# Kernel tuning notes

Measured on AMD Instinct MI355X. Metric: run time of the kernel, lower is better.

The kernel has to match this reference:

```python
import jax, jax.numpy as jnp
import numpy as np

B, T_ENC, T_OUT = 64, 1024, 1000
N_MELS, ENC_D, DEC_H, ATTN_D = 80, 256, 256, 256


def setup_inputs() -> dict:
    key = jax.random.key(0)
    ks = jax.random.split(key, 24)

    def p(k, shape, scale=0.05):
        return jax.random.normal(k, shape, dtype=jnp.float32) * scale

    lengths = jax.random.randint(ks[0], (B,), T_ENC // 2, T_ENC + 1)
    enc_mask = (jnp.arange(T_ENC)[None, :] < lengths[:, None]).astype(jnp.float32)
    return {
        "enc_outputs": jax.random.normal(ks[1], (B, T_ENC, ENC_D), dtype=jnp.float32),
        "target_mel": jax.random.normal(ks[2], (B, T_OUT, N_MELS), dtype=jnp.float32),
        # attention params
        "W_enc": p(ks[3], (ATTN_D, ENC_D)), "b_enc": jnp.zeros((ATTN_D,), jnp.float32),
        "W_dec": p(ks[4], (ATTN_D, DEC_H)), "b_dec": jnp.zeros((ATTN_D,), jnp.float32),
        "v_w": p(ks[5], (1, ATTN_D)), "v_b": jnp.zeros((1,), jnp.float32),
        # prenet
        "pre_W1": p(ks[6], (DEC_H, N_MELS)), "pre_b1": jnp.zeros((DEC_H,), jnp.float32),
        "pre_W2": p(ks[7], (DEC_H, DEC_H)), "pre_b2": jnp.zeros((DEC_H,), jnp.float32),
        # LSTMCell (PyTorch gate order i, f, g, o)
        "W_ih": p(ks[8], (4 * DEC_H, DEC_H + ENC_D)), "W_hh": p(ks[9], (4 * DEC_H, DEC_H)),
        "b_ih": jnp.zeros((4 * DEC_H,), jnp.float32), "b_hh": jnp.zeros((4 * DEC_H,), jnp.float32),
        # output heads
        "mel_W": p(ks[10], (N_MELS, DEC_H + ENC_D)), "mel_b": jnp.zeros((N_MELS,), jnp.float32),
        "stop_W": p(ks[11], (1, DEC_H + ENC_D)), "stop_b": jnp.zeros((1,), jnp.float32),
        "enc_mask": enc_mask,
    }


def reference(enc_outputs, target_mel, W_enc, b_enc, W_dec, b_dec, v_w, v_b,
              pre_W1, pre_b1, pre_W2, pre_b2, W_ih, W_hh, b_ih, b_hh,
              mel_W, mel_b, stop_W, stop_b, enc_mask):
    Bsz = enc_outputs.shape[0]
    H = W_hh.shape[1]
    NEG = jnp.float32(-1e9)
    # precompute encoder projection once, as the original does
    attn_enc = jnp.einsum('bte,ae->bta', enc_outputs, W_enc) + b_enc  # (B, T_enc, A)
    # teacher forcing: input at step t is target_mel[t-1], zeros at t=0
    prev_inputs = jnp.concatenate(
        [jnp.zeros_like(target_mel[:, :1]), target_mel[:, :-1]], axis=1)
    xs = jnp.swapaxes(prev_inputs, 0, 1)  # (T_out, B, n_mels)

    def step(carry, prev):
        h, c = carry
        attn_dec = h @ W_dec.T + b_dec                                  # (B, A)
        energy = jnp.tanh(attn_enc + attn_dec[:, None, :]) @ v_w[0] + v_b[0]  # (B, T_enc)
        energy = jnp.where(enc_mask == 0, NEG, energy)
        attn = jax.nn.softmax(energy, axis=-1)
        context = jnp.einsum('bt,btd->bd', attn, enc_outputs)           # (B, enc_d)
        pre = jax.nn.relu(prev @ pre_W1.T + pre_b1)                     # dropout = identity (eval)
        pre = jax.nn.relu(pre @ pre_W2.T + pre_b2)
        x = jnp.concatenate([pre, context], axis=1)
        gates = x @ W_ih.T + b_ih + h @ W_hh.T + b_hh                   # (B, 4H)
        i, f, g, o = jnp.split(gates, 4, axis=1)
        c_new = jax.nn.sigmoid(f) * c + jax.nn.sigmoid(i) * jnp.tanh(g)
        h_new = jax.nn.sigmoid(o) * jnp.tanh(c_new)
        comb = jnp.concatenate([h_new, context], axis=1)
        mel = comb @ mel_W.T + mel_b
        stop = (comb @ stop_W.T + stop_b)[:, 0]
        return (h_new, c_new), (mel, stop)

    h0 = jnp.zeros((Bsz, H), dtype=enc_outputs.dtype)
    _, (mels, stops) = jax.lax.scan(step, (h0, h0), xs)
    return jnp.swapaxes(mels, 0, 1), jnp.swapaxes(stops, 0, 1)
```

## Files before the change

kernel.cpp:

```cpp
#include <hip/hip_runtime.h>
#include <hip/hip_bf16.h>

#define NMEL 80

typedef unsigned u32x4 __attribute__((ext_vector_type(4)));

__device__ __forceinline__ float bf2f(unsigned short u) {
  unsigned v = ((unsigned)u) << 16; float f; __builtin_memcpy(&f, &v, 4); return f;
}
__device__ __forceinline__ unsigned short f2bf_u(float f) {
  __hip_bfloat16 h = __float2bfloat16(f); unsigned short u; __builtin_memcpy(&u, &h, 2); return u;
}
__device__ __forceinline__ void unpk(unsigned u, float& lo, float& hi) {
  unsigned l = u << 16, h = u & 0xffff0000u;
  __builtin_memcpy(&lo, &l, 4); __builtin_memcpy(&hi, &h, 4);
}

constexpr size_t OFF_ATTNR = 0;
constexpr size_t SZ_ATTNR = (size_t)64 * 1024 * 256 * 2;
constexpr size_t OFF_ENCP = OFF_ATTNR + SZ_ATTNR;
constexpr size_t SZ_ENCP = (size_t)64 * 1024 * 256 * 2;
constexpr size_t OFF_PRE2 = OFF_ENCP + SZ_ENCP;
constexpr size_t SZ_PRE2 = (size_t)64000 * 256 * 2;
constexpr size_t OFF_WDT = OFF_PRE2 + SZ_PRE2;
constexpr size_t SZ_WDT = (size_t)65536 * 4;
constexpr size_t OFF_WHT = OFF_WDT + SZ_WDT;
constexpr size_t SZ_W1M = (size_t)262144 * 4;
constexpr size_t OFF_WCT = OFF_WHT + SZ_W1M;
constexpr size_t OFF_WPT = OFF_WCT + SZ_W1M;
constexpr size_t OFF_BIASG = OFF_WPT + SZ_W1M;
constexpr size_t SZ_BIASG = 1024 * 4;
constexpr size_t WS_NEED = OFF_BIASG + SZ_BIASG;

__global__ __launch_bounds__(256) void conv_encP(const float* __restrict__ enc,
                                                 u32x4* __restrict__ encP) {
  int idx = blockIdx.x * 256 + threadIdx.x;
  int b = idx >> 15, r = idx & 32767;
  int d8 = r >> 10, te = r & 1023;
  const float4* src = (const float4*)(enc + ((size_t)(b * 1024 + te)) * 256 + d8 * 8);
  float4 x0 = src[0], x1 = src[1];
  u32x4 o;
  o.x = (unsigned)f2bf_u(x0.x) | ((unsigned)f2bf_u(x0.y) << 16);
  o.y = (unsigned)f2bf_u(x0.z) | ((unsigned)f2bf_u(x0.w) << 16);
  o.z = (unsigned)f2bf_u(x1.x) | ((unsigned)f2bf_u(x1.y) << 16);
  o.w = (unsigned)f2bf_u(x1.z) | ((unsigned)f2bf_u(x1.w) << 16);
  encP[((size_t)(b * 32 + d8)) * 1024 + te] = o;
}

__global__ __launch_bounds__(256) void prep_w2(
    const float* __restrict__ W_dec, const float* __restrict__ W_hh,
    const float* __restrict__ W_ih, const float* __restrict__ b_ih,
    const float* __restrict__ b_hh,
    float* __restrict__ WdT, float* __restrict__ WhT,
    float* __restrict__ WcT, float* __restrict__ WpT, float* __restrict__ biasG) {
  int idx = blockIdx.x * 256 + threadIdx.x;
  if (idx < 65536) {
    int q = idx & 3, a = (idx >> 2) & 255, kq = idx >> 10;
    WdT[idx] = W_dec[(size_t)a * 256 + kq * 4 + q];
  } else if (idx < 327680) {
    int i = idx - 65536;
    int q = i & 3, g = (i >> 2) & 1023, kq = i >> 12;
    WhT[i] = W_hh[(size_t)g * 256 + kq * 4 + q];
  } else if (idx < 589824) {
    int i = idx - 327680;
    int q = i & 3, g = (i >> 2) & 1023, kq = i >> 12;
    WcT[i] = W_ih[(size_t)g * 512 + 256 + kq * 4 + q];
  } else if (idx < 851968) {
    int i = idx - 589824;
    int q = i & 3, g = (i >> 2) & 1023, kq = i >> 12;
    WpT[i] = W_ih[(size_t)g * 512 + kq * 4 + q];
  } else if (idx < 852992) {
    int g = idx - 851968;
    biasG[g] = b_ih[g] + b_hh[g];
  }
}

__global__ __launch_bounds__(256) void attn_gemm(const float* __restrict__ enc,
                                                 const float* __restrict__ W_enc,
                                                 const float* __restrict__ b_enc,
                                                 unsigned* __restrict__ attnR) {
  __shared__ unsigned short Alds[64 * 260];
  const int tid = threadIdx.x;
  const int row0 = blockIdx.x * 64;
  const int wv = tid >> 6, lane = tid & 63, nb = wv * 64;
  for (int idx = tid; idx < 64 * 256; idx += 256) {
    int r = idx >> 8, k = idx & 255;
    Alds[r * 260 + k] = f2bf_u(enc[(size_t)(row0 + r) * 256 + k]);
  }
  __syncthreads();
  float acc[64];
#pragma unroll
  for (int n = 0; n < 64; ++n) acc[n] = b_enc[nb + n];
  for (int k8 = 0; k8 < 256; k8 += 8) {
    ushort4 ua = *(const ushort4*)&Alds[lane * 260 + k8];
    ushort4 ub = *(const ushort4*)&Alds[lane * 260 + k8 + 4];
    float a0 = bf2f(ua.x), a1 = bf2f(ua.y), a2 = bf2f(ua.z), a3 = bf2f(ua.w);
    float a4 = bf2f(ub.x), a5 = bf2f(ub.y), a6 = bf2f(ub.z), a7 = bf2f(ub.w);
#pragma unroll
    for (int n = 0; n < 64; ++n) {
      const float4* wp = (const float4*)(W_enc + (size_t)(nb + n) * 256 + k8);
      float4 w0 = wp[0], w1 = wp[1];
      acc[n] = fmaf(a0, w0.x, acc[n]); acc[n] = fmaf(a1, w0.y, acc[n]);
      acc[n] = fmaf(a2, w0.z, acc[n]); acc[n] = fmaf(a3, w0.w, acc[n]);
      acc[n] = fmaf(a4, w1.x, acc[n]); acc[n] = fmaf(a5, w1.y, acc[n]);
      acc[n] = fmaf(a6, w1.z, acc[n]); acc[n] = fmaf(a7, w1.w, acc[n]);
    }
  }
  const float CE = 2.8853900817779268f;
  const int b = row0 >> 10;
  const int te_g = (row0 & 1023) + lane;
  const int sl = te_g >> 8, te_loc = te_g & 255;
#pragma unroll
  for (int n = 0; n < 64; n += 2) {
    int a = nb + n;
    unsigned pair = (unsigned)f2bf_u(acc[n] * CE) | ((unsigned)f2bf_u(acc[n + 1] * CE) << 16);
    size_t u4 = ((((size_t)(b * 4 + sl) * 4 + (a >> 6)) * 8 + ((a >> 3) & 7)) * 256 + te_loc);
    attnR[u4 * 4 + ((a & 7) >> 1)] = pair;
  }
}

__global__ __launch_bounds__(256) void prenet_fused(const float* __restrict__ tmel,
                                                    const float* __restrict__ W1,
                                                    const float* __restrict__ b1,
                                                    const float* __restrict__ W2,
                                                    const float* __restrict__ b2,
                                                    unsigned short* __restrict__ pre2) {
  __shared__ unsigned short Alds[64 * 260];
  const int tid = threadIdx.x;
  const int row0 = blockIdx.x * 64;
  const int wv = tid >> 6, lane = tid & 63, nb = wv * 64;
  for (int idx = tid; idx < 64 * 80; idx += 256) {
    int r = idx / 80, k = idx - r * 80;
    int R = row0 + r;
    float v = (R % 1000 != 0) ? tmel[(size_t)(R - 1) * NMEL + k] : 0.f;
    Alds[r * 260 + k] = f2bf_u(v);
  }
  __syncthreads();
  float acc[64];
#pragma unroll
  for (int n = 0; n < 64; ++n) acc[n] = b1[nb + n];
  for (int k8 = 0; k8 < 80; k8 += 8) {
    ushort4 ua = *(const ushort4*)&Alds[lane * 260 + k8];
    ushort4 ub = *(const ushort4*)&Alds[lane * 260 + k8 + 4];
    float a0 = bf2f(ua.x), a1 = bf2f(ua.y), a2 = bf2f(ua.z), a3 = bf2f(ua.w);
    float a4 = bf2f(ub.x), a5 = bf2f(ub.y), a6 = bf2f(ub.z), a7 = bf2f(ub.w);
#pragma unroll
    for (int n = 0; n < 64; ++n) {
      const float4* wp = (const float4*)(W1 + (size_t)(nb + n) * 80 + k8);
      float4 w0 = wp[0], w1 = wp[1];
      acc[n] = fmaf(a0, w0.x, acc[n]); acc[n] = fmaf(a1, w0.y, acc[n]);
      acc[n] = fmaf(a2, w0.z, acc[n]); acc[n] = fmaf(a3, w0.w, acc[n]);
      acc[n] = fmaf(a4, w1.x, acc[n]); acc[n] = fmaf(a5, w1.y, acc[n]);
      acc[n] = fmaf(a6, w1.z, acc[n]); acc[n] = fmaf(a7, w1.w, acc[n]);
    }
  }
  __syncthreads();
#pragma unroll
  for (int n = 0; n < 64; ++n) Alds[lane * 260 + nb + n] = f2bf_u(fmaxf(acc[n], 0.f));
  __syncthreads();
#pragma unroll
  for (int n = 0; n < 64; ++n) acc[n] = b2[nb + n];
  for (int k8 = 0; k8 < 256; k8 += 8) {
    ushort4 ua = *(const ushort4*)&Alds[lane * 260 + k8];
    ushort4 ub = *(const ushort4*)&Alds[lane * 260 + k8 + 4];
    float a0 = bf2f(ua.x), a1 = bf2f(ua.y), a2 = bf2f(ua.z), a3 = bf2f(ua.w);
    float a4 = bf2f(ub.x), a5 = bf2f(ub.y), a6 = bf2f(ub.z), a7 = bf2f(ub.w);
#pragma unroll
    for (int n = 0; n < 64; ++n) {
      const float4* wp = (const float4*)(W2 + (size_t)(nb + n) * 256 + k8);
      float4 w0 = wp[0], w1 = wp[1];
      acc[n] = fmaf(a0, w0.x, acc[n]); acc[n] = fmaf(a1, w0.y, acc[n]);
      acc[n] = fmaf(a2, w0.z, acc[n]); acc[n] = fmaf(a3, w0.w, acc[n]);
      acc[n] = fmaf(a4, w1.x, acc[n]); acc[n] = fmaf(a5, w1.y, acc[n]);
      acc[n] = fmaf(a6, w1.z, acc[n]); acc[n] = fmaf(a7, w1.w, acc[n]);
    }
  }
  __syncthreads();
#pragma unroll
  for (int n = 0; n < 64; ++n) Alds[lane * 260 + nb + n] = f2bf_u(fmaxf(acc[n], 0.f));
  __syncthreads();
  for (int idx = tid; idx < 64 * 128; idx += 256) {
    int r = idx >> 7, k2 = (idx & 127) * 2;
    unsigned pair = (unsigned)Alds[r * 260 + k2] | ((unsigned)Alds[r * 260 + k2 + 1] << 16);
    *(unsigned*)(pre2 + (size_t)(row0 + r) * 256 + k2) = pair;
  }
}

__global__ __launch_bounds__(1024, 1) void decoder_one(
    const u32x4* __restrict__ attnR, const u32x4* __restrict__ encP,
    const unsigned short* __restrict__ pre2,
    const float4* __restrict__ WdT, const float4* __restrict__ WhT,
    const float4* __restrict__ WcT, const float4* __restrict__ WpT,
    const float* __restrict__ biasG,
    const float* __restrict__ b_dec, const float* __restrict__ v_w,
    const float* __restrict__ v_b, const float* __restrict__ enc_mask,
    const float* __restrict__ mel_W, const float* __restrict__ mel_b,
    const float* __restrict__ stop_W, const float* __restrict__ stop_b,
    float* __restrict__ out) {
  __shared__ __align__(16) float scratchB[8448];
  __shared__ __align__(16) float p_lds[1024];
  __shared__ __align__(16) float gates_lds[1024];
  __shared__ __align__(16) float h_lds[256];
  __shared__ __align__(16) float ctx_lds[256];
  __shared__ __align__(16) float pre_lds[256];
  __shared__ __align__(16) float dec_lds[256];
  __shared__ __align__(16) float v2_lds[256];
  __shared__ float red_lds[16];

  const int tid = threadIdx.x;
  const int b = blockIdx.x;
  const int t8 = tid & 255, chunk = tid >> 8;
  const int lane = tid & 63, wid = tid >> 6;
  const int d8 = tid >> 5, tec = tid & 31;
  const float CE = 2.8853900817779268f;
  const float L2E = 1.4426950408889634f;

  if (tid < 256) {
    h_lds[tid] = 0.f;
    float v = v_w[tid];
    v2_lds[tid] = -2.f * v;
    for (int m = 32; m; m >>= 1) v += __shfl_xor(v, m);
    if (lane == 0) red_lds[wid] = v;
  }
  float c_reg = 0.f;
  const float maskv = enc_mask[b * 1024 + tid];
  const float bdec_r = (tid < 256) ? b_dec[tid] : 0.f;
  const float biasg_r = biasG[tid];
  const float melb_r = (tid < 640 && (tid & 7) == 0) ? mel_b[tid >> 3] : 0.f;
  float stopw[8];
  if (wid == 11) {
#pragma unroll
    for (int i = 0; i < 8; ++i) stopw[i] = stop_W[lane * 8 + i];
  }
  __syncthreads();
  const float Sv_vb = red_lds[0] + red_lds[1] + red_lds[2] + red_lds[3] + v_b[0];
  const float stopb0 = stop_b[0];

  const u32x4* aB = attnR + (size_t)b * 32768 + chunk * 2048 + t8;
  const u32x4* eB = encP + ((size_t)(b * 32 + d8)) * 1024 + tec;
  const float4* wdB = WdT + chunk * 16 * 256 + t8;
  const float4* whB = WhT + tid;
  const float4* wcB = WcT + tid;
  const float4* wpB = WpT + tid;
  const unsigned short* pre2_b = pre2 + (size_t)b * 256000;
  float* outm = out + (size_t)b * 80000;
  float* outs = out + (size_t)5120000 + b * 1000;

  auto heads = [&](int ith) {
    if (tid < 640) {
      const int m = tid >> 3, q = tid & 7;
      float acc = melb_r;
      const float4* wm = (const float4*)(mel_W + (size_t)m * 512 + q * 64);
      const float4* xp = (q < 4) ? (const float4*)&h_lds[q * 64]
                                 : (const float4*)&ctx_lds[(q - 4) * 64];
#pragma unroll
      for (int i = 0; i < 16; ++i) {
        float4 w = wm[i]; float4 x = xp[i];
        acc = fmaf(w.x, x.x, acc); acc = fmaf(w.y, x.y, acc);
        acc = fmaf(w.z, x.z, acc); acc = fmaf(w.w, x.w, acc);
      }
      acc += __shfl_xor(acc, 1); acc += __shfl_xor(acc, 2); acc += __shfl_xor(acc, 4);
      if (q == 0) outm[ith * 80 + m] = acc;
    } else if (wid == 11) {
      float acc = 0.f;
#pragma unroll
      for (int i = 0; i < 8; ++i) {
        int cc = lane * 8 + i;
        float x = (cc < 256) ? h_lds[cc] : ctx_lds[cc - 256];
        acc = fmaf(stopw[i], x, acc);
      }
      for (int m = 32; m; m >>= 1) acc += __shfl_xor(acc, m);
      if (lane == 0) outs[ith] = acc + stopb0;
    }
  };

  float gph = 0.f;

  for (int it = 0; it < 1000; ++it) {
    {
      float acc = 0.f;
#pragma unroll
      for (int i = 0; i < 16; ++i) {
        float4 w = wdB[(size_t)i << 8];
        float4 h4 = *(const float4*)&h_lds[chunk * 64 + i * 4];
        acc = fmaf(w.x, h4.x, acc); acc = fmaf(w.y, h4.y, acc);
        acc = fmaf(w.z, h4.z, acc); acc = fmaf(w.w, h4.w, acc);
      }
      scratchB[(chunk << 8) + t8] = acc;
      if (tid < 256) pre_lds[tid] = bf2f(pre2_b[it * 256 + tid]);
      if (it > 0) heads(it - 1);
    }
    __syncthreads();
    if (tid < 256)
      dec_lds[tid] = (bdec_r + scratchB[tid] + scratchB[256 + tid] +
                      scratchB[512 + tid] + scratchB[768 + tid]) * CE;
    __syncthreads();
#pragma unroll 1
    for (int sl = 0; sl < 4; ++sl) {
      float acc = 0.f;
#pragma unroll
      for (int j = 0; j < 8; ++j) {
        u32x4 u = __builtin_nontemporal_load(&aB[sl * 8192 + j * 256]);
        int ab = (chunk << 6) + (j << 3);
        float4 d0 = *(const float4*)&dec_lds[ab];
        float4 d1 = *(const float4*)&dec_lds[ab + 4];
        float4 v0 = *(const float4*)&v2_lds[ab];
        float4 v1 = *(const float4*)&v2_lds[ab + 4];
        float t0, t1, t2, t3, t4, t5, t6, t7;
        unpk(u.x, t0, t1); unpk(u.y, t2, t3); unpk(u.z, t4, t5); unpk(u.w, t6, t7);
        acc = fmaf(v0.x, __builtin_amdgcn_rcpf(1.f + __builtin_amdgcn_exp2f(t0 + d0.x)), acc);
        acc = fmaf(v0.y, __builtin_amdgcn_rcpf(1.f + __builtin_amdgcn_exp2f(t1 + d0.y)), acc);
        acc = fmaf(v0.z, __builtin_amdgcn_rcpf(1.f + __builtin_amdgcn_exp2f(t2 + d0.z)), acc);
        acc = fmaf(v0.w, __builtin_amdgcn_rcpf(1.f + __builtin_amdgcn_exp2f(t3 + d0.w)), acc);
        acc = fmaf(v1.x, __builtin_amdgcn_rcpf(1.f + __builtin_amdgcn_exp2f(t4 + d1.x)), acc);
        acc = fmaf(v1.y, __builtin_amdgcn_rcpf(1.f + __builtin_amdgcn_exp2f(t5 + d1.y)), acc);
        acc = fmaf(v1.z, __builtin_amdgcn_rcpf(1.f + __builtin_amdgcn_exp2f(t6 + d1.z)), acc);
        acc = fmaf(v1.w, __builtin_amdgcn_rcpf(1.f + __builtin_amdgcn_exp2f(t7 + d1.w)), acc);
      }
      scratchB[sl * 1024 + (chunk << 8) + t8] = acc;
    }
    __syncthreads();
    {
      int base = (tid >> 8) * 1024 + (tid & 255);
      float e = Sv_vb + scratchB[base] + scratchB[base + 256] +
                scratchB[base + 512] + scratchB[base + 768];
      float p = (maskv != 0.f) ? __builtin_amdgcn_exp2f(e * L2E) : 0.f;
      p_lds[tid] = p;
      for (int m = 32; m; m >>= 1) p += __shfl_xor(p, m);
      if (lane == 0) red_lds[wid] = p;
    }
    __syncthreads();
    {
      gph = biasg_r;
      float cc0 = 0, cc1 = 0, cc2 = 0, cc3 = 0, cc4 = 0, cc5 = 0, cc6 = 0, cc7 = 0;
      u32x4 eb[8];
      auto issueQ = [&](int q0) {
#pragma unroll
        for (int t = 0; t < 8; ++t)
          eb[t] = __builtin_nontemporal_load(&eB[((q0 << 3) + t) << 5]);
      };
      auto consumeQ = [&](int q0) {
#pragma unroll
        for (int t = 0; t < 8; ++t) {
          float pv = p_lds[((((q0 << 3) + t) << 5)) + tec];
          float e0, e1, e2, e3, e4, e5, e6, e7;
          unpk(eb[t].x, e0, e1); unpk(eb[t].y, e2, e3);
          unpk(eb[t].z, e4, e5); unpk(eb[t].w, e6, e7);
          cc0 = fmaf(pv, e0, cc0); cc1 = fmaf(pv, e1, cc1);
          cc2 = fmaf(pv, e2, cc2); cc3 = fmaf(pv, e3, cc3);
          cc4 = fmaf(pv, e4, cc4); cc5 = fmaf(pv, e5, cc5);
          cc6 = fmaf(pv, e6, cc6); cc7 = fmaf(pv, e7, cc7);
        }
      };
      auto gdot = [&](const float4* __restrict__ wB, const float* __restrict__ xl, int i0) {
#pragma unroll 8
        for (int i = i0; i < i0 + 32; ++i) {
          float4 w = wB[(size_t)i << 10];
          float4 x = *(const float4*)&xl[i << 2];
          gph = fmaf(w.x, x.x, gph); gph = fmaf(w.y, x.y, gph);
          gph = fmaf(w.z, x.z, gph); gph = fmaf(w.w, x.w, gph);
        }
      };
      issueQ(0); gdot(wpB, pre_lds, 0);  consumeQ(0);
      issueQ(1); gdot(wpB, pre_lds, 32); consumeQ(1);
      issueQ(2); gdot(whB, h_lds, 0);    consumeQ(2);
      issueQ(3); gdot(whB, h_lds, 32);   consumeQ(3);
      float* cb = &scratchB[(d8 << 3) * 33 + tec];
      cb[0] = cc0; cb[33] = cc1; cb[66] = cc2; cb[99] = cc3;
      cb[132] = cc4; cb[165] = cc5; cb[198] = cc6; cb[231] = cc7;
    }
    __syncthreads();
    if (tid < 256) {
      float S = red_lds[0] + red_lds[1] + red_lds[2] + red_lds[3] +
                red_lds[4] + red_lds[5] + red_lds[6] + red_lds[7] +
                red_lds[8] + red_lds[9] + red_lds[10] + red_lds[11] +
                red_lds[12] + red_lds[13] + red_lds[14] + red_lds[15];
      float rS = 1.f / S;
      float s = 0.f;
      const float* row = &scratchB[tid * 33];
#pragma unroll
      for (int t = 0; t < 32; ++t) s += row[t];
      ctx_lds[tid] = s * rS;
    }
    __syncthreads();
    {
      float g = gph;
#pragma unroll 8
      for (int i = 0; i < 64; ++i) {
        float4 w = wcB[(size_t)i << 10];
        float4 x = *(const float4*)&ctx_lds[i << 2];
        g = fmaf(w.x, x.x, g); g = fmaf(w.y, x.y, g);
        g = fmaf(w.z, x.z, g); g = fmaf(w.w, x.w, g);
      }
      gates_lds[tid] = g;
    }
    __syncthreads();
    if (tid < 256) {
      float ii = gates_lds[tid], ff = gates_lds[256 + tid];
      float gg = gates_lds[512 + tid], oo = gates_lds[768 + tid];
      float si = __builtin_amdgcn_rcpf(1.f + __builtin_amdgcn_exp2f(-ii * L2E));
      float sf = __builtin_amdgcn_rcpf(1.f + __builtin_amdgcn_exp2f(-ff * L2E));
      float so = __builtin_amdgcn_rcpf(1.f + __builtin_amdgcn_exp2f(-oo * L2E));
      float tg2 = 1.f - 2.f * __builtin_amdgcn_rcpf(1.f + __builtin_amdgcn_exp2f(gg * CE));
      float cn = sf * c_reg + si * tg2;
      float tc = 1.f - 2.f * __builtin_amdgcn_rcpf(1.f + __builtin_amdgcn_exp2f(cn * CE));
      c_reg = cn;
      h_lds[tid] = so * tc;
    }
    __syncthreads();
  }
  heads(999);
}

extern "C" void kernel_launch(void* const* d_in, const int* in_sizes, int n_in,
                              void* d_out, int out_size, void* d_ws, size_t ws_size,
                              hipStream_t stream) {
  const float* enc = (const float*)d_in[0];
  const float* tmel = (const float*)d_in[1];
  const float* W_enc = (const float*)d_in[2];
  const float* b_enc = (const float*)d_in[3];
  const float* W_dec = (const float*)d_in[4];
  const float* b_dec = (const float*)d_in[5];
  const float* v_w = (const float*)d_in[6];
  const float* v_b = (const float*)d_in[7];
  const float* pW1 = (const float*)d_in[8];
  const float* pb1 = (const float*)d_in[9];
  const float* pW2 = (const float*)d_in[10];
  const float* pb2 = (const float*)d_in[11];
  const float* W_ih = (const float*)d_in[12];
  const float* W_hh = (const float*)d_in[13];
  const float* b_ih = (const float*)d_in[14];
  const float* b_hh = (const float*)d_in[15];
  const float* mel_W = (const float*)d_in[16];
  const float* mel_b = (const float*)d_in[17];
  const float* stop_W = (const float*)d_in[18];
  const float* stop_b = (const float*)d_in[19];
  const float* emask = (const float*)d_in[20];

  if (ws_size < WS_NEED) return;

  char* ws = (char*)d_ws;
  unsigned* attnR = (unsigned*)(ws + OFF_ATTNR);
  u32x4* encP = (u32x4*)(ws + OFF_ENCP);
  unsigned short* pre2 = (unsigned short*)(ws + OFF_PRE2);
  float* WdT = (float*)(ws + OFF_WDT);
  float* WhT = (float*)(ws + OFF_WHT);
  float* WcT = (float*)(ws + OFF_WCT);
  float* WpT = (float*)(ws + OFF_WPT);
  float* biasG = (float*)(ws + OFF_BIASG);

  conv_encP<<<8192, 256, 0, stream>>>(enc, encP);
  prep_w2<<<3332, 256, 0, stream>>>(W_dec, W_hh, W_ih, b_ih, b_hh, WdT, WhT, WcT, WpT, biasG);
  attn_gemm<<<1024, 256, 0, stream>>>(enc, W_enc, b_enc, attnR);
  prenet_fused<<<1000, 256, 0, stream>>>(tmel, pW1, pb1, pW2, pb2, pre2);
  decoder_one<<<64, 1024, 0, stream>>>(
      (const u32x4*)attnR, (const u32x4*)encP, pre2,
      (const float4*)WdT, (const float4*)WhT, (const float4*)WcT, (const float4*)WpT,
      biasG, b_dec, v_w, v_b, emask, mel_W, mel_b, stop_W, stop_b, (float*)d_out);
}
```

Measured before the change: 176.1 ms.

## Halve decoder block to 512 threads with two work items per thread

The persistent decoder kernel drops from 1024 to 512 threads per block, and each thread now handles two halves of every stage: attention energies, context accumulation, gate dot products and the mel head. Loads for both halves are issued together to raise memory-level parallelism, and there are fewer waves to synchronise at each barrier. The cost is more registers and serial work per thread and fewer waves to hide latency, with only 64 blocks on the GPU.

```diff
diff --git a/kernel.cpp b/kernel.cpp
--- a/kernel.cpp
+++ b/kernel.cpp
@@ -186,7 +186,7 @@
   }
 }
 
-__global__ __launch_bounds__(1024, 1) void decoder_one(
+__global__ __launch_bounds__(512, 2) void decoder_one(
     const u32x4* __restrict__ attnR, const u32x4* __restrict__ encP,
     const unsigned short* __restrict__ pre2,
     const float4* __restrict__ WdT, const float4* __restrict__ WhT,
@@ -223,12 +223,14 @@
     if (lane == 0) red_lds[wid] = v;
   }
   float c_reg = 0.f;
-  const float maskv = enc_mask[b * 1024 + tid];
+  const float maskv0 = enc_mask[b * 1024 + tid];
+  const float maskv1 = enc_mask[b * 1024 + 512 + tid];
   const float bdec_r = (tid < 256) ? b_dec[tid] : 0.f;
-  const float biasg_r = biasG[tid];
-  const float melb_r = (tid < 640 && (tid & 7) == 0) ? mel_b[tid >> 3] : 0.f;
+  const float biasg0 = biasG[tid];
+  const float biasg1 = biasG[512 + tid];
+  const float melb_r = (tid < 320 && (tid & 3) == 0) ? mel_b[tid >> 2] : 0.f;
   float stopw[8];
-  if (wid == 11) {
+  if (wid == 7) {
 #pragma unroll
     for (int i = 0; i < 8; ++i) stopw[i] = stop_W[lane * 8 + i];
   }
@@ -237,8 +239,8 @@
   const float stopb0 = stop_b[0];
 
   const u32x4* aB = attnR + (size_t)b * 32768 + chunk * 2048 + t8;
-  const u32x4* eB = encP + ((size_t)(b * 32 + d8)) * 1024 + tec;
-  const float4* wdB = WdT + chunk * 16 * 256 + t8;
+  const u32x4* eB0 = encP + ((size_t)(b * 32 + d8)) * 1024 + tec;
+  const float4* wdB = WdT + (size_t)(chunk * 32) * 256 + t8;
   const float4* whB = WhT + tid;
   const float4* wcB = WcT + tid;
   const float4* wpB = WpT + tid;
@@ -247,21 +249,21 @@
   float* outs = out + (size_t)5120000 + b * 1000;
 
   auto heads = [&](int ith) {
-    if (tid < 640) {
-      const int m = tid >> 3, q = tid & 7;
+    if (tid < 320) {
+      const int m = tid >> 2, q = tid & 3;
       float acc = melb_r;
-      const float4* wm = (const float4*)(mel_W + (size_t)m * 512 + q * 64);
-      const float4* xp = (q < 4) ? (const float4*)&h_lds[q * 64]
-                                 : (const float4*)&ctx_lds[(q - 4) * 64];
-#pragma unroll
-      for (int i = 0; i < 16; ++i) {
+      const float4* wm = (const float4*)(mel_W + (size_t)m * 512 + q * 128);
+      const float4* xp = (q < 2) ? (const float4*)&h_lds[q * 128]
+                                 : (const float4*)&ctx_lds[(q - 2) * 128];
+#pragma unroll 8
+      for (int i = 0; i < 32; ++i) {
         float4 w = wm[i]; float4 x = xp[i];
         acc = fmaf(w.x, x.x, acc); acc = fmaf(w.y, x.y, acc);
         acc = fmaf(w.z, x.z, acc); acc = fmaf(w.w, x.w, acc);
       }
-      acc += __shfl_xor(acc, 1); acc += __shfl_xor(acc, 2); acc += __shfl_xor(acc, 4);
+      acc += __shfl_xor(acc, 1); acc += __shfl_xor(acc, 2);
       if (q == 0) outm[ith * 80 + m] = acc;
-    } else if (wid == 11) {
+    } else if (wid == 7) {
       float acc = 0.f;
 #pragma unroll
       for (int i = 0; i < 8; ++i) {
@@ -274,15 +276,15 @@
     }
   };
 
-  float gph = 0.f;
+  float gph0 = 0.f, gph1 = 0.f;
 
   for (int it = 0; it < 1000; ++it) {
     {
       float acc = 0.f;
-#pragma unroll
-      for (int i = 0; i < 16; ++i) {
+#pragma unroll 8
+      for (int i = 0; i < 32; ++i) {
         float4 w = wdB[(size_t)i << 8];
-        float4 h4 = *(const float4*)&h_lds[chunk * 64 + i * 4];
+        float4 h4 = *(const float4*)&h_lds[chunk * 128 + i * 4];
         acc = fmaf(w.x, h4.x, acc); acc = fmaf(w.y, h4.y, acc);
         acc = fmaf(w.z, h4.z, acc); acc = fmaf(w.w, h4.w, acc);
       }
@@ -292,89 +294,144 @@
     }
     __syncthreads();
     if (tid < 256)
-      dec_lds[tid] = (bdec_r + scratchB[tid] + scratchB[256 + tid] +
-                      scratchB[512 + tid] + scratchB[768 + tid]) * CE;
+      dec_lds[tid] = (bdec_r + scratchB[tid] + scratchB[256 + tid]) * CE;
     __syncthreads();
 #pragma unroll 1
     for (int sl = 0; sl < 4; ++sl) {
-      float acc = 0.f;
+      u32x4 ua[8], ub[8];
+#pragma unroll
+      for (int j = 0; j < 8; ++j) ua[j] = __builtin_nontemporal_load(&aB[sl * 8192 + j * 256]);
+#pragma unroll
+      for (int j = 0; j < 8; ++j)
+        ub[j] = __builtin_nontemporal_load(&aB[4096 + sl * 8192 + j * 256]);
+      float acc0 = 0.f, acc1 = 0.f;
 #pragma unroll
       for (int j = 0; j < 8; ++j) {
-        u32x4 u = __builtin_nontemporal_load(&aB[sl * 8192 + j * 256]);
         int ab = (chunk << 6) + (j << 3);
         float4 d0 = *(const float4*)&dec_lds[ab];
         float4 d1 = *(const float4*)&dec_lds[ab + 4];
         float4 v0 = *(const float4*)&v2_lds[ab];
         float4 v1 = *(const float4*)&v2_lds[ab + 4];
         float t0, t1, t2, t3, t4, t5, t6, t7;
-        unpk(u.x, t0, t1); unpk(u.y, t2, t3); unpk(u.z, t4, t5); unpk(u.w, t6, t7);
-        acc = fmaf(v0.x, __builtin_amdgcn_rcpf(1.f + __builtin_amdgcn_exp2f(t0 + d0.x)), acc);
-        acc = fmaf(v0.y, __builtin_amdgcn_rcpf(1.f + __builtin_amdgcn_exp2f(t1 + d0.y)), acc);
-        acc = fmaf(v0.z, __builtin_amdgcn_rcpf(1.f + __builtin_amdgcn_exp2f(t2 + d0.z)), acc);
-        acc = fmaf(v0.w, __builtin_amdgcn_rcpf(1.f + __builtin_amdgcn_exp2f(t3 + d0.w)), acc);
-        acc = fmaf(v1.x, __builtin_amdgcn_rcpf(1.f + __builtin_amdgcn_exp2f(t4 + d1.x)), acc);
-        acc = fmaf(v1.y, __builtin_amdgcn_rcpf(1.f + __builtin_amdgcn_exp2f(t5 + d1.y)), acc);
-        acc = fmaf(v1.z, __builtin_amdgcn_rcpf(1.f + __builtin_amdgcn_exp2f(t6 + d1.z)), acc);
-        acc = fmaf(v1.w, __builtin_amdgcn_rcpf(1.f + __builtin_amdgcn_exp2f(t7 + d1.w)), acc);
-      }
-      scratchB[sl * 1024 + (chunk << 8) + t8] = acc;
+        unpk(ua[j].x, t0, t1); unpk(ua[j].y, t2, t3);
+        unpk(ua[j].z, t4, t5); unpk(ua[j].w, t6, t7);
+        acc0 = fmaf(v0.x, __builtin_amdgcn_rcpf(1.f + __builtin_amdgcn_exp2f(t0 + d0.x)), acc0);
+        acc0 = fmaf(v0.y, __builtin_amdgcn_rcpf(1.f + __builtin_amdgcn_exp2f(t1 + d0.y)), acc0);
+        acc0 = fmaf(v0.z, __builtin_amdgcn_rcpf(1.f + __builtin_amdgcn_exp2f(t2 + d0.z)), acc0);
+        acc0 = fmaf(v0.w, __builtin_amdgcn_rcpf(1.f + __builtin_amdgcn_exp2f(t3 + d0.w)), acc0);
+        acc0 = fmaf(v1.x, __builtin_amdgcn_rcpf(1.f + __builtin_amdgcn_exp2f(t4 + d1.x)), acc0);
+        acc0 = fmaf(v1.y, __builtin_amdgcn_rcpf(1.f + __builtin_amdgcn_exp2f(t5 + d1.y)), acc0);
+        acc0 = fmaf(v1.z, __builtin_amdgcn_rcpf(1.f + __builtin_amdgcn_exp2f(t6 + d1.z)), acc0);
+        acc0 = fmaf(v1.w, __builtin_amdgcn_rcpf(1.f + __builtin_amdgcn_exp2f(t7 + d1.w)), acc0);
+      }
+#pragma unroll
+      for (int j = 0; j < 8; ++j) {
+        int ab = (chunk << 6) + (j << 3) + 128;
+        float4 d0 = *(const float4*)&dec_lds[ab];
+        float4 d1 = *(const float4*)&dec_lds[ab + 4];
+        float4 v0 = *(const float4*)&v2_lds[ab];
+        float4 v1 = *(const float4*)&v2_lds[ab + 4];
+        float t0, t1, t2, t3, t4, t5, t6, t7;
+        unpk(ub[j].x, t0, t1); unpk(ub[j].y, t2, t3);
+        unpk(ub[j].z, t4, t5); unpk(ub[j].w, t6, t7);
+        acc1 = fmaf(v0.x, __builtin_amdgcn_rcpf(1.f + __builtin_amdgcn_exp2f(t0 + d0.x)), acc1);
+        acc1 = fmaf(v0.y, __builtin_amdgcn_rcpf(1.f + __builtin_amdgcn_exp2f(t1 + d0.y)), acc1);
+        acc1 = fmaf(v0.z, __builtin_amdgcn_rcpf(1.f + __builtin_amdgcn_exp2f(t2 + d0.z)), acc1);
+        acc1 = fmaf(v0.w, __builtin_amdgcn_rcpf(1.f + __builtin_amdgcn_exp2f(t3 + d0.w)), acc1);
+        acc1 = fmaf(v1.x, __builtin_amdgcn_rcpf(1.f + __builtin_amdgcn_exp2f(t4 + d1.x)), acc1);
+        acc1 = fmaf(v1.y, __builtin_amdgcn_rcpf(1.f + __builtin_amdgcn_exp2f(t5 + d1.y)), acc1);
+        acc1 = fmaf(v1.z, __builtin_amdgcn_rcpf(1.f + __builtin_amdgcn_exp2f(t6 + d1.z)), acc1);
+        acc1 = fmaf(v1.w, __builtin_amdgcn_rcpf(1.f + __builtin_amdgcn_exp2f(t7 + d1.w)), acc1);
+      }
+      scratchB[sl * 1024 + (chunk << 8) + t8] = acc0;
+      scratchB[sl * 1024 + ((chunk + 2) << 8) + t8] = acc1;
     }
     __syncthreads();
     {
       int base = (tid >> 8) * 1024 + (tid & 255);
-      float e = Sv_vb + scratchB[base] + scratchB[base + 256] +
-                scratchB[base + 512] + scratchB[base + 768];
-      float p = (maskv != 0.f) ? __builtin_amdgcn_exp2f(e * L2E) : 0.f;
-      p_lds[tid] = p;
-      for (int m = 32; m; m >>= 1) p += __shfl_xor(p, m);
-      if (lane == 0) red_lds[wid] = p;
+      float e0 = Sv_vb + scratchB[base] + scratchB[base + 256] +
+                 scratchB[base + 512] + scratchB[base + 768];
+      float e1 = Sv_vb + scratchB[base + 2048] + scratchB[base + 2304] +
+                 scratchB[base + 2560] + scratchB[base + 2816];
+      float p0 = (maskv0 != 0.f) ? __builtin_amdgcn_exp2f(e0 * L2E) : 0.f;
+      float p1 = (maskv1 != 0.f) ? __builtin_amdgcn_exp2f(e1 * L2E) : 0.f;
+      p_lds[tid] = p0;
+      p_lds[tid + 512] = p1;
+      float sp = p0 + p1;
+      for (int m = 32; m; m >>= 1) sp += __shfl_xor(sp, m);
+      if (lane == 0) red_lds[wid] = sp;
     }
     __syncthreads();
     {
-      gph = biasg_r;
-      float cc0 = 0, cc1 = 0, cc2 = 0, cc3 = 0, cc4 = 0, cc5 = 0, cc6 = 0, cc7 = 0;
-      u32x4 eb[8];
-      auto issueQ = [&](int q0) {
+      gph0 = biasg0; gph1 = biasg1;
+      float cA0 = 0, cA1 = 0, cA2 = 0, cA3 = 0, cA4 = 0, cA5 = 0, cA6 = 0, cA7 = 0;
+      float cB0 = 0, cB1 = 0, cB2 = 0, cB3 = 0, cB4 = 0, cB5 = 0, cB6 = 0, cB7 = 0;
+      u32x4 ea[8], eb2[8];
+#pragma unroll
+      for (int q = 0; q < 4; ++q) {
+        const float4* wB = (q < 2) ? wpB : whB;
+        const float* xl = (q < 2) ? pre_lds : h_lds;
+        const int k0 = (q & 1) * 32;
 #pragma unroll
         for (int t = 0; t < 8; ++t)
-          eb[t] = __builtin_nontemporal_load(&eB[((q0 << 3) + t) << 5]);
-      };
-      auto consumeQ = [&](int q0) {
+          ea[t] = __builtin_nontemporal_load(&eB0[(q * 8 + t) << 5]);
+#pragma unroll 8
+        for (int i = k0; i < k0 + 16; ++i) {
+          float4 w0 = wB[(size_t)i << 10];
+          float4 w1 = wB[((size_t)i << 10) + 512];
+          float4 x = *(const float4*)&xl[i << 2];
+          gph0 = fmaf(w0.x, x.x, gph0); gph0 = fmaf(w0.y, x.y, gph0);
+          gph0 = fmaf(w0.z, x.z, gph0); gph0 = fmaf(w0.w, x.w, gph0);
+          gph1 = fmaf(w1.x, x.x, gph1); gph1 = fmaf(w1.y, x.y, gph1);
+          gph1 = fmaf(w1.z, x.z, gph1); gph1 = fmaf(w1.w, x.w, gph1);
+        }
 #pragma unroll
         for (int t = 0; t < 8; ++t) {
-          float pv = p_lds[((((q0 << 3) + t) << 5)) + tec];
+          float pv = p_lds[((q * 8 + t) << 5) + tec];
           float e0, e1, e2, e3, e4, e5, e6, e7;
-          unpk(eb[t].x, e0, e1); unpk(eb[t].y, e2, e3);
-          unpk(eb[t].z, e4, e5); unpk(eb[t].w, e6, e7);
-          cc0 = fmaf(pv, e0, cc0); cc1 = fmaf(pv, e1, cc1);
-          cc2 = fmaf(pv, e2, cc2); cc3 = fmaf(pv, e3, cc3);
-          cc4 = fmaf(pv, e4, cc4); cc5 = fmaf(pv, e5, cc5);
-          cc6 = fmaf(pv, e6, cc6); cc7 = fmaf(pv, e7, cc7);
+          unpk(ea[t].x, e0, e1); unpk(ea[t].y, e2, e3);
+          unpk(ea[t].z, e4, e5); unpk(ea[t].w, e6, e7);
+          cA0 = fmaf(pv, e0, cA0); cA1 = fmaf(pv, e1, cA1);
+          cA2 = fmaf(pv, e2, cA2); cA3 = fmaf(pv, e3, cA3);
+          cA4 = fmaf(pv, e4, cA4); cA5 = fmaf(pv, e5, cA5);
+          cA6 = fmaf(pv, e6, cA6); cA7 = fmaf(pv, e7, cA7);
         }
-      };
-      auto gdot = [&](const float4* __restrict__ wB, const float* __restrict__ xl, int i0) {
+#pragma unroll
+        for (int t = 0; t < 8; ++t)
+          eb2[t] = __builtin_nontemporal_load(&eB0[16384 + ((q * 8 + t) << 5)]);
 #pragma unroll 8
-        for (int i = i0; i < i0 + 32; ++i) {
-          float4 w = wB[(size_t)i << 10];
+        for (int i = k0 + 16; i < k0 + 32; ++i) {
+          float4 w0 = wB[(size_t)i << 10];
+          float4 w1 = wB[((size_t)i << 10) + 512];
           float4 x = *(const float4*)&xl[i << 2];
-          gph = fmaf(w.x, x.x, gph); gph = fmaf(w.y, x.y, gph);
-          gph = fmaf(w.z, x.z, gph); gph = fmaf(w.w, x.w, gph);
+          gph0 = fmaf(w0.x, x.x, gph0); gph0 = fmaf(w0.y, x.y, gph0);
+          gph0 = fmaf(w0.z, x.z, gph0); gph0 = fmaf(w0.w, x.w, gph0);
+          gph1 = fmaf(w1.x, x.x, gph1); gph1 = fmaf(w1.y, x.y, gph1);
+          gph1 = fmaf(w1.z, x.z, gph1); gph1 = fmaf(w1.w, x.w, gph1);
         }
-      };
-      issueQ(0); gdot(wpB, pre_lds, 0);  consumeQ(0);
-      issueQ(1); gdot(wpB, pre_lds, 32); consumeQ(1);
-      issueQ(2); gdot(whB, h_lds, 0);    consumeQ(2);
-      issueQ(3); gdot(whB, h_lds, 32);   consumeQ(3);
-      float* cb = &scratchB[(d8 << 3) * 33 + tec];
-      cb[0] = cc0; cb[33] = cc1; cb[66] = cc2; cb[99] = cc3;
-      cb[132] = cc4; cb[165] = cc5; cb[198] = cc6; cb[231] = cc7;
+#pragma unroll
+        for (int t = 0; t < 8; ++t) {
+          float pv = p_lds[((q * 8 + t) << 5) + tec];
+          float e0, e1, e2, e3, e4, e5, e6, e7;
+          unpk(eb2[t].x, e0, e1); unpk(eb2[t].y, e2, e3);
+          unpk(eb2[t].z, e4, e5); unpk(eb2[t].w, e6, e7);
+          cB0 = fmaf(pv, e0, cB0); cB1 = fmaf(pv, e1, cB1);
+          cB2 = fmaf(pv, e2, cB2); cB3 = fmaf(pv, e3, cB3);
+          cB4 = fmaf(pv, e4, cB4); cB5 = fmaf(pv, e5, cB5);
+          cB6 = fmaf(pv, e6, cB6); cB7 = fmaf(pv, e7, cB7);
+        }
+      }
+      float* cb0 = &scratchB[(d8 << 3) * 33 + tec];
+      cb0[0] = cA0; cb0[33] = cA1; cb0[66] = cA2; cb0[99] = cA3;
+      cb0[132] = cA4; cb0[165] = cA5; cb0[198] = cA6; cb0[231] = cA7;
+      float* cb1 = &scratchB[((d8 + 16) << 3) * 33 + tec];
+      cb1[0] = cB0; cb1[33] = cB1; cb1[66] = cB2; cb1[99] = cB3;
+      cb1[132] = cB4; cb1[165] = cB5; cb1[198] = cB6; cb1[231] = cB7;
     }
     __syncthreads();
     if (tid < 256) {
       float S = red_lds[0] + red_lds[1] + red_lds[2] + red_lds[3] +
-                red_lds[4] + red_lds[5] + red_lds[6] + red_lds[7] +
-                red_lds[8] + red_lds[9] + red_lds[10] + red_lds[11] +
-                red_lds[12] + red_lds[13] + red_lds[14] + red_lds[15];
+                red_lds[4] + red_lds[5] + red_lds[6] + red_lds[7];
       float rS = 1.f / S;
       float s = 0.f;
       const float* row = &scratchB[tid * 33];
@@ -384,15 +441,19 @@
     }
     __syncthreads();
     {
-      float g = gph;
+      float g0 = gph0, g1 = gph1;
 #pragma unroll 8
       for (int i = 0; i < 64; ++i) {
-        float4 w = wcB[(size_t)i << 10];
+        float4 w0 = wcB[(size_t)i << 10];
+        float4 w1 = wcB[((size_t)i << 10) + 512];
         float4 x = *(const float4*)&ctx_lds[i << 2];
-        g = fmaf(w.x, x.x, g); g = fmaf(w.y, x.y, g);
-        g = fmaf(w.z, x.z, g); g = fmaf(w.w, x.w, g);
-      }
-      gates_lds[tid] = g;
+        g0 = fmaf(w0.x, x.x, g0); g0 = fmaf(w0.y, x.y, g0);
+        g0 = fmaf(w0.z, x.z, g0); g0 = fmaf(w0.w, x.w, g0);
+        g1 = fmaf(w1.x, x.x, g1); g1 = fmaf(w1.y, x.y, g1);
+        g1 = fmaf(w1.z, x.z, g1); g1 = fmaf(w1.w, x.w, g1);
+      }
+      gates_lds[tid] = g0;
+      gates_lds[tid + 512] = g1;
     }
     __syncthreads();
     if (tid < 256) {
@@ -453,7 +514,7 @@
   prep_w2<<<3332, 256, 0, stream>>>(W_dec, W_hh, W_ih, b_ih, b_hh, WdT, WhT, WcT, WpT, biasG);
   attn_gemm<<<1024, 256, 0, stream>>>(enc, W_enc, b_enc, attnR);
   prenet_fused<<<1000, 256, 0, stream>>>(tmel, pW1, pb1, pW2, pb2, pre2);
-  decoder_one<<<64, 1024, 0, stream>>>(
+  decoder_one<<<64, 512, 0, stream>>>(
       (const u32x4*)attnR, (const u32x4*)encP, pre2,
       (const float4*)WdT, (const float4*)WhT, (const float4*)WcT, (const float4*)WpT,
       biasG, b_dec, v_w, v_b, emask, mel_W, mel_b, stop_W, stop_b, (float*)d_out);
```

New measurement: 267.2 ms. 1.52x slower.

## Shrink LDS scratch, reduce context via shuffles, restructure attention and context load pipelines

Applied to the files above, without the earlier changes.

Cuts the scratch LDS buffer from 8448 to 4096 floats and drops the min-blocks launch bound. The 32-way tec reduction of context partials now uses wave shuffles into a small ctxp buffer instead of a padded LDS transpose. The energy loop issues all eight loads up front per slice and adds a barrier per slice. The context loop becomes an 8-stage software pipeline with 4-load double buffering, interleaved with smaller gate-dot chunks. The aim is lower LDS traffic and better latency hiding, at the cost of extra barriers and different register pressure in this one-block-per-batch recurrent kernel.

```diff
diff --git a/kernel.cpp b/kernel.cpp
--- a/kernel.cpp
+++ b/kernel.cpp
@@ -186,7 +186,7 @@
   }
 }
 
-__global__ __launch_bounds__(1024, 1) void decoder_one(
+__global__ __launch_bounds__(1024) void decoder_one(
     const u32x4* __restrict__ attnR, const u32x4* __restrict__ encP,
     const unsigned short* __restrict__ pre2,
     const float4* __restrict__ WdT, const float4* __restrict__ WhT,
@@ -197,11 +197,12 @@
     const float* __restrict__ mel_W, const float* __restrict__ mel_b,
     const float* __restrict__ stop_W, const float* __restrict__ stop_b,
     float* __restrict__ out) {
-  __shared__ __align__(16) float scratchB[8448];
+  __shared__ __align__(16) float scratchB[4096];
   __shared__ __align__(16) float p_lds[1024];
   __shared__ __align__(16) float gates_lds[1024];
   __shared__ __align__(16) float h_lds[256];
   __shared__ __align__(16) float ctx_lds[256];
+  __shared__ __align__(16) float ctxp_lds[256];
   __shared__ __align__(16) float pre_lds[256];
   __shared__ __align__(16) float dec_lds[256];
   __shared__ __align__(16) float v2_lds[256];
@@ -295,12 +296,8 @@
       dec_lds[tid] = (bdec_r + scratchB[tid] + scratchB[256 + tid] +
                       scratchB[512 + tid] + scratchB[768 + tid]) * CE;
     __syncthreads();
-#pragma unroll 1
-    for (int sl = 0; sl < 4; ++sl) {
-      float acc = 0.f;
-#pragma unroll
-      for (int j = 0; j < 8; ++j) {
-        u32x4 u = __builtin_nontemporal_load(&aB[sl * 8192 + j * 256]);
+    {
+      auto consume = [&](u32x4 u, int j, float& acc) {
         int ab = (chunk << 6) + (j << 3);
         float4 d0 = *(const float4*)&dec_lds[ab];
         float4 d1 = *(const float4*)&dec_lds[ab + 4];
@@ -316,10 +313,25 @@
         acc = fmaf(v1.y, __builtin_amdgcn_rcpf(1.f + __builtin_amdgcn_exp2f(t5 + d1.y)), acc);
         acc = fmaf(v1.z, __builtin_amdgcn_rcpf(1.f + __builtin_amdgcn_exp2f(t6 + d1.z)), acc);
         acc = fmaf(v1.w, __builtin_amdgcn_rcpf(1.f + __builtin_amdgcn_exp2f(t7 + d1.w)), acc);
-      }
-      scratchB[sl * 1024 + (chunk << 8) + t8] = acc;
-    }
-    __syncthreads();
+      };
+#pragma unroll 1
+      for (int sl = 0; sl < 4; ++sl) {
+        const u32x4* ap = aB + sl * 8192;
+        u32x4 u0 = __builtin_nontemporal_load(&ap[0 * 256]);
+        u32x4 u1 = __builtin_nontemporal_load(&ap[1 * 256]);
+        u32x4 u2 = __builtin_nontemporal_load(&ap[2 * 256]);
+        u32x4 u3 = __builtin_nontemporal_load(&ap[3 * 256]);
+        u32x4 u4 = __builtin_nontemporal_load(&ap[4 * 256]);
+        u32x4 u5 = __builtin_nontemporal_load(&ap[5 * 256]);
+        u32x4 u6 = __builtin_nontemporal_load(&ap[6 * 256]);
+        u32x4 u7 = __builtin_nontemporal_load(&ap[7 * 256]);
+        float acc = 0.f;
+        consume(u0, 0, acc); consume(u1, 1, acc); consume(u2, 2, acc); consume(u3, 3, acc);
+        consume(u4, 4, acc); consume(u5, 5, acc); consume(u6, 6, acc); consume(u7, 7, acc);
+        scratchB[sl * 1024 + (chunk << 8) + t8] = acc;
+        __syncthreads();
+      }
+    }
     {
       int base = (tid >> 8) * 1024 + (tid & 255);
       float e = Sv_vb + scratchB[base] + scratchB[base + 256] +
@@ -333,41 +345,55 @@
     {
       gph = biasg_r;
       float cc0 = 0, cc1 = 0, cc2 = 0, cc3 = 0, cc4 = 0, cc5 = 0, cc6 = 0, cc7 = 0;
-      u32x4 eb[8];
-      auto issueQ = [&](int q0) {
-#pragma unroll
-        for (int t = 0; t < 8; ++t)
-          eb[t] = __builtin_nontemporal_load(&eB[((q0 << 3) + t) << 5]);
+      auto cons = [&](u32x4 u, int s) {
+        float pv = p_lds[(s << 5) + tec];
+        float e0, e1, e2, e3, e4, e5, e6, e7;
+        unpk(u.x, e0, e1); unpk(u.y, e2, e3);
+        unpk(u.z, e4, e5); unpk(u.w, e6, e7);
+        cc0 = fmaf(pv, e0, cc0); cc1 = fmaf(pv, e1, cc1);
+        cc2 = fmaf(pv, e2, cc2); cc3 = fmaf(pv, e3, cc3);
+        cc4 = fmaf(pv, e4, cc4); cc5 = fmaf(pv, e5, cc5);
+        cc6 = fmaf(pv, e6, cc6); cc7 = fmaf(pv, e7, cc7);
       };
-      auto consumeQ = [&](int q0) {
-#pragma unroll
-        for (int t = 0; t < 8; ++t) {
-          float pv = p_lds[((((q0 << 3) + t) << 5)) + tec];
-          float e0, e1, e2, e3, e4, e5, e6, e7;
-          unpk(eb[t].x, e0, e1); unpk(eb[t].y, e2, e3);
-          unpk(eb[t].z, e4, e5); unpk(eb[t].w, e6, e7);
-          cc0 = fmaf(pv, e0, cc0); cc1 = fmaf(pv, e1, cc1);
-          cc2 = fmaf(pv, e2, cc2); cc3 = fmaf(pv, e3, cc3);
-          cc4 = fmaf(pv, e4, cc4); cc5 = fmaf(pv, e5, cc5);
-          cc6 = fmaf(pv, e6, cc6); cc7 = fmaf(pv, e7, cc7);
+      u32x4 e0 = __builtin_nontemporal_load(&eB[0 << 5]);
+      u32x4 e1 = __builtin_nontemporal_load(&eB[1 << 5]);
+      u32x4 e2 = __builtin_nontemporal_load(&eB[2 << 5]);
+      u32x4 e3 = __builtin_nontemporal_load(&eB[3 << 5]);
+#pragma unroll
+      for (int g = 0; g < 8; ++g) {
+        {
+          const float4* wB = (g < 4) ? wpB : whB;
+          const float* xl = (g < 4) ? pre_lds : h_lds;
+          const int i0 = (g & 3) * 16;
+#pragma unroll
+          for (int i = i0; i < i0 + 16; ++i) {
+            float4 w = wB[(size_t)i << 10];
+            float4 x = *(const float4*)&xl[i << 2];
+            gph = fmaf(w.x, x.x, gph); gph = fmaf(w.y, x.y, gph);
+            gph = fmaf(w.z, x.z, gph); gph = fmaf(w.w, x.w, gph);
+          }
         }
-      };
-      auto gdot = [&](const float4* __restrict__ wB, const float* __restrict__ xl, int i0) {
-#pragma unroll 8
-        for (int i = i0; i < i0 + 32; ++i) {
-          float4 w = wB[(size_t)i << 10];
-          float4 x = *(const float4*)&xl[i << 2];
-          gph = fmaf(w.x, x.x, gph); gph = fmaf(w.y, x.y, gph);
-          gph = fmaf(w.z, x.z, gph); gph = fmaf(w.w, x.w, gph);
+        u32x4 c0 = e0, c1 = e1, c2 = e2, c3 = e3;
+        if (g < 7) {
+          const int s = g * 4 + 4;
+          e0 = __builtin_nontemporal_load(&eB[(s + 0) << 5]);
+          e1 = __builtin_nontemporal_load(&eB[(s + 1) << 5]);
+          e2 = __builtin_nontemporal_load(&eB[(s + 2) << 5]);
+          e3 = __builtin_nontemporal_load(&eB[(s + 3) << 5]);
         }
-      };
-      issueQ(0); gdot(wpB, pre_lds, 0);  consumeQ(0);
-      issueQ(1); gdot(wpB, pre_lds, 32); consumeQ(1);
-      issueQ(2); gdot(whB, h_lds, 0);    consumeQ(2);
-      issueQ(3); gdot(whB, h_lds, 32);   consumeQ(3);
-      float* cb = &scratchB[(d8 << 3) * 33 + tec];
-      cb[0] = cc0; cb[33] = cc1; cb[66] = cc2; cb[99] = cc3;
-      cb[132] = cc4; cb[165] = cc5; cb[198] = cc6; cb[231] = cc7;
+        cons(c0, g * 4 + 0); cons(c1, g * 4 + 1);
+        cons(c2, g * 4 + 2); cons(c3, g * 4 + 3);
+      }
+#define REDTEC(x) { x += __shfl_xor(x, 1); x += __shfl_xor(x, 2); x += __shfl_xor(x, 4); \
+                    x += __shfl_xor(x, 8); x += __shfl_xor(x, 16); }
+      REDTEC(cc0) REDTEC(cc1) REDTEC(cc2) REDTEC(cc3)
+      REDTEC(cc4) REDTEC(cc5) REDTEC(cc6) REDTEC(cc7)
+#undef REDTEC
+      if (tec == 0) {
+        float* cp = &ctxp_lds[d8 << 3];
+        cp[0] = cc0; cp[1] = cc1; cp[2] = cc2; cp[3] = cc3;
+        cp[4] = cc4; cp[5] = cc5; cp[6] = cc6; cp[7] = cc7;
+      }
     }
     __syncthreads();
     if (tid < 256) {
@@ -375,12 +401,7 @@
                 red_lds[4] + red_lds[5] + red_lds[6] + red_lds[7] +
                 red_lds[8] + red_lds[9] + red_lds[10] + red_lds[11] +
                 red_lds[12] + red_lds[13] + red_lds[14] + red_lds[15];
-      float rS = 1.f / S;
-      float s = 0.f;
-      const float* row = &scratchB[tid * 33];
-#pragma unroll
-      for (int t = 0; t < 32; ++t) s += row[t];
-      ctx_lds[tid] = s * rS;
+      ctx_lds[tid] = ctxp_lds[tid] * (1.f / S);
     }
     __syncthreads();
     {
```

After: 305.6 ms. 1.74x slower.
